# Kernel optimization log

Measured on AMD Instinct MI355X. Metric: run time of the kernel, lower is better.

Reference implementation:

```python
import jax, jax.numpy as jnp
import numpy as np

B, T = 256, 25
PRE = 2048   # resnet feature dim
D = 256      # fc_early_dim = cell_size = in_size = hybrid_in_size
K = 4        # num_atts
NC = 2       # num_classes


def setup_inputs() -> dict:
    key = jax.random.key(0)
    ks = jax.random.split(key, 20)
    def p(k, *s):
        return jax.random.normal(k, s, jnp.float32) * 0.02
    z = lambda *s: jnp.zeros(s, jnp.float32)
    return {
        "x_visual": jax.random.normal(ks[0], (B, T, PRE), jnp.float32),
        "x_tactile": jax.random.normal(ks[1], (B, T, PRE), jnp.float32),
        "fc0_w": p(ks[2], PRE, D), "fc0_b": z(D),
        "fc1_w": p(ks[3], PRE, D), "fc1_b": z(D),
        # LSTHM_V: W(x) + U(h) + V(z), gates packed as [f,i,o,ch]
        "lv_W": p(ks[4], D, 4 * D), "lv_U": p(ks[5], D, 4 * D), "lv_V": p(ks[6], D, 4 * D), "lv_b": z(4 * D),
        # LSTHM_T
        "lt_W": p(ks[7], D, 4 * D), "lt_U": p(ks[8], D, 4 * D), "lt_V": p(ks[9], D, 4 * D), "lt_b": z(4 * D),
        # MAB: attention over concat hidden (2D) producing K attentions
        "att_w": p(ks[10], 2 * D, K * 2 * D), "att_b": z(K * 2 * D),
        "red_v_w": p(ks[11], K * D, D), "red_v_b": z(D),
        "red_t_w": p(ks[12], K * D, D), "red_t_b": z(D),
        "mab_out_w": p(ks[13], 2 * D, D), "mab_out_b": z(D),
        "late0_w": p(ks[14], 2 * D, D), "late0_b": z(D),
        "late1_w": p(ks[15], D, NC), "late1_b": z(NC),
    }


def _lsthm(x, c, h, zz, W, U, V, b):
    s = x @ W + h @ U + zz @ V + b            # [B, 4D]
    f = jax.nn.sigmoid(s[:, :D])
    i = jax.nn.sigmoid(s[:, D:2 * D])
    o = jax.nn.sigmoid(s[:, 2 * D:3 * D])
    ch = jnp.tanh(s[:, 3 * D:])
    c_new = f * c + i * ch
    return c_new, jnp.tanh(c_new) * o


def reference(x_visual, x_tactile, fc0_w, fc0_b, fc1_w, fc1_b,
              lv_W, lv_U, lv_V, lv_b, lt_W, lt_U, lt_V, lt_b,
              att_w, att_b, red_v_w, red_v_b, red_t_w, red_t_b,
              mab_out_w, mab_out_b, late0_w, late0_b, late1_w, late1_b):
    xv = x_visual @ fc0_w + fc0_b             # [B, T, D]
    xt = x_tactile @ fc1_w + fc1_b            # [B, T, D]

    def mab(h_v, h_t):
        h = jnp.concatenate([h_v, h_t], -1)   # [B, 2D]
        att = jax.nn.softmax(h @ att_w + att_b, axis=-1)       # [B, K*2D]
        attd = att.reshape(-1, K, 2 * D) * h[:, None, :]        # K attended copies
        v = attd[:, :, :D].reshape(-1, K * D)
        t = attd[:, :, D:].reshape(-1, K * D)
        rv = jax.nn.relu(v @ red_v_w + red_v_b)
        rt = jax.nn.relu(t @ red_t_w + red_t_b)
        return jnp.concatenate([rv, rt], -1) @ mab_out_w + mab_out_b  # [B, D]

    def step(carry, xs):
        c_v, h_v, c_t, h_t, zz = carry
        xvi, xti = xs
        c_v, h_v = _lsthm(xvi, c_v, h_v, zz, lv_W, lv_U, lv_V, lv_b)
        c_t, h_t = _lsthm(xti, c_t, h_t, zz, lt_W, lt_U, lt_V, lt_b)
        zz = mab(h_v, h_t)
        return (c_v, h_v, c_t, h_t, zz), None

    zeros = jnp.zeros((x_visual.shape[0], D), jnp.float32)
    init = (zeros, zeros, zeros, zeros, zeros)
    (c_v, h_v, c_t, h_t, zz), _ = jax.lax.scan(
        step, init, (jnp.swapaxes(xv, 0, 1), jnp.swapaxes(xt, 0, 1)))
    x = jnp.concatenate([h_v, h_t], -1) @ late0_w + late0_b
    return x @ late1_w + late1_b              # dropout is identity in eval
```

## Files before the change

### kernel.cpp

```cpp
#include <hip/hip_runtime.h>

typedef unsigned short u16;
typedef unsigned int u32;
typedef unsigned long long u64;
using bfrag = __attribute__((ext_vector_type(8))) short;
using facc  = __attribute__((ext_vector_type(4))) float;

#define DEV __device__ __forceinline__
#define AGT __HIP_MEMORY_SCOPE_AGENT

static constexpr size_t o_xv   = 0;
static constexpr size_t o_xt   = 3276800;
static constexpr size_t o_f0T  = 6553600;
static constexpr size_t o_f1T  = 7602176;
static constexpr size_t o_UVWv = 8650752;
static constexpr size_t o_UVWt = 10747904;
static constexpr size_t o_attT = 12845056;
static constexpr size_t o_redT = 14942208;
static constexpr size_t o_bgv  = 15990784;
static constexpr size_t o_bgt  = 15994880;
static constexpr size_t o_mvv  = 15998976;
static constexpr size_t o_mvt  = 16003072;
static constexpr size_t o_FW   = 16007168;
static constexpr size_t o_fb   = 16011264;
static constexpr size_t o_eh   = 16011520;
static constexpr size_t o_psum = 41177344;
static constexpr size_t o_hv   = 42750208;
static constexpr size_t o_ht   = 46158080;
static constexpr size_t o_rvt  = 49565952;
static constexpr size_t o_bar  = 56119552;
static constexpr size_t o_end  = 56135936;

DEV u16 f2bf(float f) {
    u32 u = __float_as_uint(f);
    u32 r = (u + 0x7FFFu + ((u >> 16) & 1u)) >> 16;
    return (u16)r;
}
DEV float bf2f(u16 h) { return __uint_as_float(((u32)h) << 16); }
DEV u32 pk2(float a, float b) { return (u32)f2bf(a) | ((u32)f2bf(b) << 16); }
DEV float sigm(float x) { return 1.0f / (1.0f + __expf(-x)); }
DEV float tanh2(float x) { return 2.0f * sigm(2.0f * x) - 1.0f; }
DEV facc mfma16(bfrag a, bfrag b, facc c) {
    return __builtin_amdgcn_mfma_f32_16x16x32_bf16(a, b, c, 0, 0, 0);
}

DEV void gbar(u32* flags, int b, u32 k) {
    asm volatile("s_waitcnt vmcnt(0)" ::: "memory");
    __syncthreads();
    if (threadIdx.x == 0) {
        __builtin_amdgcn_fence(__ATOMIC_RELEASE, "agent");
        (void)__hip_atomic_exchange(&flags[b * 16], k, __ATOMIC_RELAXED, AGT);
    }
    u32* myf = &flags[threadIdx.x * 16];
    while (__hip_atomic_load(myf, __ATOMIC_RELAXED, AGT) < k)
        __builtin_amdgcn_s_sleep(1);
    __syncthreads();
}


DEV void prep_T(const float* __restrict__ src, u16* dst, int lgK, int N, int nb, int bl, int tid) {
    int pairs = ((1 << lgK) * N) >> 1;
    int kmask = (1 << lgK) - 1;
    for (int idx = bl * 256 + tid; idx < pairs; idx += nb * 256) {
        int i = idx * 2;
        int n = i >> lgK, k = i & kmask;
        *(u32*)&dst[i] = pk2(src[(size_t)k * N + n], src[(size_t)(k + 1) * N + n]);
    }
}

DEV void prep_UVW(const float* U, const float* mo, const float* V, const float* W,
                  u16* dst, int nb, int bl, int tid) {
    for (int idx = bl * 256 + tid; idx < 1024 * 1024; idx += nb * 256) {
        int p = idx >> 10, k = idx & 1023;
        int j = p >> 2, g = p & 3, gc = g * 256 + j;
        float v;
        if (k < 256) v = U[(size_t)k * 1024 + gc];
        else if (k < 768) {
            int s = k - 256;
            float a = 0.f;
            for (int d = 0; d < 256; ++d) a += mo[s * 256 + d] * V[(size_t)d * 1024 + gc];
            v = a;
        } else v = W[(size_t)(k - 768) * 1024 + gc];
        dst[idx] = f2bf(v);
    }
}

DEV void prep_bias(const float* lb, const float* mob, const float* V,
                   float* bg, float* mv, int nb, int bl, int tid) {
    for (int p = bl * 256 + tid; p < 1024; p += nb * 256) {
        int j = p >> 2, g = p & 3, gc = g * 256 + j;
        bg[p] = lb[gc];
        float a = 0.f;
        for (int d = 0; d < 256; ++d) a += mob[d] * V[(size_t)d * 1024 + gc];
        mv[p] = a;
    }
}

DEV void prep_FW(const float* l0w, const float* l0b, const float* l1w, const float* l1b,
                 float* FW, float* fb, int tid) {
    for (int idx = tid; idx < 1024; idx += 256) {
        int k = idx >> 1, c = idx & 1;
        float a = 0.f;
        for (int j = 0; j < 256; ++j) a += l0w[k * 256 + j] * l1w[j * 2 + c];
        FW[idx] = a;
    }
    if (tid < 2) {
        float a = l1b[tid];
        for (int j = 0; j < 256; ++j) a += l0b[j] * l1w[j * 2 + tid];
        fb[tid] = a;
    }
}

struct KP { const float* in[26]; char* ws; float* out; };

__global__ __launch_bounds__(256) void marn_all(KP P) {
    __shared__ __align__(16) unsigned char SM[31744];
    int tid = threadIdx.x, b = blockIdx.x;
    int w = tid >> 6, l = tid & 63, lm = l & 15, kh = l >> 4;
    u32 bk = 0;
    char* ws = P.ws;

    u16* xv = (u16*)(ws + o_xv);
    u16* xt = (u16*)(ws + o_xt);
    u16* f0T = (u16*)(ws + o_f0T);
    u16* f1T = (u16*)(ws + o_f1T);
    u16* UVWv = (u16*)(ws + o_UVWv);
    u16* UVWt = (u16*)(ws + o_UVWt);
    u16* attT = (u16*)(ws + o_attT);
    u16* redT = (u16*)(ws + o_redT);
    float* bgv = (float*)(ws + o_bgv);
    float* bgt = (float*)(ws + o_bgt);
    float* mvv = (float*)(ws + o_mvv);
    float* mvt = (float*)(ws + o_mvt);
    float* FW = (float*)(ws + o_FW);
    float* fb = (float*)(ws + o_fb);
    u16* ehB = (u16*)(ws + o_eh);
    float* psB = (float*)(ws + o_psum);
    u16* hvB = (u16*)(ws + o_hv);
    u16* htB = (u16*)(ws + o_ht);
    u16* rvB = (u16*)(ws + o_rvt);
    u32* bar = (u32*)(ws + o_bar);
    const float* attb = P.in[15];
    const float* rvb = P.in[17];
    const float* rtb = P.in[19];

    if      (b < 24)  prep_T(P.in[2], f0T, 11, 256, 24, b, tid);
    else if (b < 48)  prep_T(P.in[4], f1T, 11, 256, 24, b - 24, tid);
    else if (b < 96)  prep_T(P.in[14], attT, 9, 2048, 48, b - 48, tid);
    else if (b < 108) prep_T(P.in[16], redT, 10, 256, 12, b - 96, tid);
    else if (b < 120) prep_T(P.in[18], redT + 256 * 1024, 10, 256, 12, b - 108, tid);
    else if (b < 176) prep_UVW(P.in[7], P.in[20], P.in[8], P.in[6], UVWv, 56, b - 120, tid);
    else if (b < 232) prep_UVW(P.in[11], P.in[20], P.in[12], P.in[10], UVWt, 56, b - 176, tid);
    else if (b < 236) prep_bias(P.in[9], P.in[21], P.in[8], bgv, mvv, 4, b - 232, tid);
    else if (b < 240) prep_bias(P.in[13], P.in[21], P.in[12], bgt, mvt, 4, b - 236, tid);
    else if (b == 240) prep_FW(P.in[22], P.in[23], P.in[24], P.in[25], FW, fb, tid);
    gbar(bar, b, ++bk);

    {
        u16* Al = (u16*)SM;
        u16* Bl = (u16*)(SM + 9216);
        u16* Lt = (u16*)SM;
        for (int u = b; u < 400; u += 256) {
            int zs = u & 1, ny = (u >> 1) & 1, mx = u >> 2;
            const float* A = zs ? P.in[1] : P.in[0];
            const u16* BT = zs ? f1T : f0T;
            const float* bias = zs ? P.in[5] : P.in[3];
            u16* C = zs ? xt : xv;
            int m0 = mx * 64, n0 = ny * 128;
            int arow = tid >> 2, aseg = tid & 3;
            int brow = tid >> 1, bseg = tid & 1;
            facc acc[8];
#pragma unroll
            for (int i = 0; i < 8; ++i) acc[i] = (facc){0.f, 0.f, 0.f, 0.f};
            for (int c = 0; c < 32; ++c) {
                float4 av[4];
#pragma unroll
                for (int uu = 0; uu < 4; ++uu)
                    av[uu] = *(const float4*)&A[(size_t)(m0 + arow) * 2048 + c * 64 + aseg * 16 + uu * 4];
                uint4 bv[4];
#pragma unroll
                for (int uu = 0; uu < 4; ++uu)
                    bv[uu] = *(const uint4*)&BT[(size_t)(n0 + brow) * 2048 + c * 64 + bseg * 32 + uu * 8];
                __syncthreads();
                u32 pk[8];
#pragma unroll
                for (int uu = 0; uu < 4; ++uu) {
                    pk[2 * uu] = pk2(av[uu].x, av[uu].y);
                    pk[2 * uu + 1] = pk2(av[uu].z, av[uu].w);
                }
                *(uint4*)&Al[arow * 72 + aseg * 16] = make_uint4(pk[0], pk[1], pk[2], pk[3]);
                *(uint4*)&Al[arow * 72 + aseg * 16 + 8] = make_uint4(pk[4], pk[5], pk[6], pk[7]);
#pragma unroll
                for (int uu = 0; uu < 4; ++uu)
                    *(uint4*)&Bl[brow * 72 + bseg * 32 + uu * 8] = bv[uu];
                __syncthreads();
#pragma unroll
                for (int ks = 0; ks < 2; ++ks) {
                    bfrag a = *(const bfrag*)&Al[(16 * w + lm) * 72 + ks * 32 + kh * 8];
#pragma unroll
                    for (int tt = 0; tt < 8; ++tt) {
                        bfrag bb = *(const bfrag*)&Bl[(tt * 16 + lm) * 72 + ks * 32 + kh * 8];
                        acc[tt] = mfma16(a, bb, acc[tt]);
                    }
                }
            }
            __syncthreads();
#pragma unroll
            for (int tt = 0; tt < 8; ++tt)
#pragma unroll
                for (int j = 0; j < 4; ++j)
                    Lt[(16 * w + 4 * kh + j) * 128 + tt * 16 + lm] = f2bf(acc[tt][j] + bias[n0 + tt * 16 + lm]);
            __syncthreads();
            {
                int mloc = tid >> 2, seg = tid & 3;
                int mg = m0 + mloc;
                int bi = mg / 25, ti = mg - bi * 25;
                u16* drow = &C[(size_t)(ti * 256 + bi) * 256 + n0 + seg * 32];
                const uint4* lp = (const uint4*)&Lt[mloc * 128 + seg * 32];
#pragma unroll
                for (int i = 0; i < 4; ++i)
                    *(uint4*)&drow[i * 8] = lp[i];
            }
            __syncthreads();
        }
    }
    gbar(bar, b, ++bk);

    float* sscr = (float*)SM;
    float* ppart = (float*)(SM + 26112);
    float* sinvl = (float*)(SM + 27136);
    float* redscr = (float*)(SM + 27200);
    float creg[2] = {0.f, 0.f};
    int xid = b & 7, q = b >> 3;

    for (int t = 0; t < 25; ++t) {
        const u16* hv_t = hvB + t * 65536;
        const u16* ht_t = htB + t * 65536;
        u16* hv_n = hvB + (t + 1) * 65536;
        u16* ht_n = htB + (t + 1) * 65536;
        const u16* rv_t = rvB + t * 131072;

        {
            int m = q & 3, n = xid * 8 + (q >> 2);
            int r0 = m * 64;
            bool sv = (n < 32);
            int p0 = (sv ? n : n - 32) * 32;
            const u16* UVW = sv ? UVWv : UVWt;
            const u16* hb = sv ? hv_t : ht_t;
            const u16* xb = (sv ? xv : xt) + t * 65536;
            int arow = r0 + 16 * w + lm;
            const u16* Ah = hb + arow * 256 + kh * 8;
            const u16* Ar = rv_t + arow * 512 + kh * 8;
            const u16* Ax = xb + arow * 256 + kh * 8;
            const u16* B0 = UVW + (size_t)(p0 + lm) * 1024 + kh * 8;
            const u16* B1 = UVW + (size_t)(p0 + 16 + lm) * 1024 + kh * 8;
            facc acc0 = (facc){0.f, 0.f, 0.f, 0.f}, acc1 = (facc){0.f, 0.f, 0.f, 0.f};
#pragma unroll
            for (int ks = 0; ks < 8; ++ks) {
                bfrag a = *(const bfrag*)(Ah + ks * 32);
                bfrag b0 = *(const bfrag*)(B0 + ks * 32);
                bfrag b1 = *(const bfrag*)(B1 + ks * 32);
                acc0 = mfma16(a, b0, acc0);
                acc1 = mfma16(a, b1, acc1);
            }
#pragma unroll
            for (int ks = 0; ks < 16; ++ks) {
                bfrag a = *(const bfrag*)(Ar + ks * 32);
                bfrag b0 = *(const bfrag*)(B0 + 256 + ks * 32);
                bfrag b1 = *(const bfrag*)(B1 + 256 + ks * 32);
                acc0 = mfma16(a, b0, acc0);
                acc1 = mfma16(a, b1, acc1);
            }
#pragma unroll
            for (int ks = 0; ks < 8; ++ks) {
                bfrag a = *(const bfrag*)(Ax + ks * 32);
                bfrag b0 = *(const bfrag*)(B0 + 768 + ks * 32);
                bfrag b1 = *(const bfrag*)(B1 + 768 + ks * 32);
                acc0 = mfma16(a, b0, acc0);
                acc1 = mfma16(a, b1, acc1);
            }
            __syncthreads();
#pragma unroll
            for (int j = 0; j < 4; ++j) {
                sscr[(16 * w + 4 * kh + j) * 33 + lm] = acc0[j];
                sscr[(16 * w + 4 * kh + j) * 33 + 16 + lm] = acc1[j];
            }
            __syncthreads();
            const float* bg = sv ? bgv : bgt;
            const float* mv = sv ? mvv : mvt;
            float tf = (t > 0) ? 1.0f : 0.0f;
            int r = tid >> 2, jp = tid & 3;
            float h2[2];
#pragma unroll
            for (int e = 0; e < 2; ++e) {
                int p = jp * 8 + e * 4;
                float4 b4 = *(const float4*)&bg[p0 + p];
                float4 m4 = *(const float4*)&mv[p0 + p];
                float s0 = sscr[r * 33 + p + 0] + b4.x + tf * m4.x;
                float s1 = sscr[r * 33 + p + 1] + b4.y + tf * m4.y;
                float s2 = sscr[r * 33 + p + 2] + b4.z + tf * m4.z;
                float s3 = sscr[r * 33 + p + 3] + b4.w + tf * m4.w;
                float fg = sigm(s0), ig = sigm(s1), og = sigm(s2), ch = tanh2(s3);
                float cn = fg * creg[e] + ig * ch;
                creg[e] = cn;
                h2[e] = tanh2(cn) * og;
            }
            u16* hw = sv ? hv_n : ht_n;
            *(u32*)&hw[(r0 + r) * 256 + (p0 >> 2) + jp * 2] = pk2(h2[0], h2[1]);
        }
        gbar(bar, b, ++bk);

        if (t < 24) {
            u16* eh_t = ehB + (size_t)t * 524288;
            float* ps_t = psB + t * 16384;

            {
                int m = q & 3, n = xid * 8 + (q >> 2);
                int r0 = m * 64, c0 = n * 32;
                int arow = r0 + 16 * w + lm;
                const u16* A0 = hv_n + arow * 256 + kh * 8;
                const u16* A1 = ht_n + arow * 256 + kh * 8;
                const u16* B0 = attT + (size_t)(c0 + lm) * 512 + kh * 8;
                const u16* B1 = attT + (size_t)(c0 + 16 + lm) * 512 + kh * 8;
                facc acc0 = (facc){0.f, 0.f, 0.f, 0.f}, acc1 = (facc){0.f, 0.f, 0.f, 0.f};
#pragma unroll
                for (int ks = 0; ks < 8; ++ks) {
                    bfrag a = *(const bfrag*)(A0 + ks * 32);
                    bfrag b0 = *(const bfrag*)(B0 + ks * 32);
                    bfrag b1 = *(const bfrag*)(B1 + ks * 32);
                    acc0 = mfma16(a, b0, acc0);
                    acc1 = mfma16(a, b1, acc1);
                }
#pragma unroll
                for (int ks = 0; ks < 8; ++ks) {
                    bfrag a = *(const bfrag*)(A1 + ks * 32);
                    bfrag b0 = *(const bfrag*)(B0 + 256 + ks * 32);
                    bfrag b1 = *(const bfrag*)(B1 + 256 + ks * 32);
                    acc0 = mfma16(a, b0, acc0);
                    acc1 = mfma16(a, b1, acc1);
                }
                __syncthreads();
#pragma unroll
                for (int j = 0; j < 4; ++j) {
                    sscr[(16 * w + 4 * kh + j) * 33 + lm] = acc0[j];
                    sscr[(16 * w + 4 * kh + j) * 33 + 16 + lm] = acc1[j];
                }
                __syncthreads();
                int r = tid >> 2, qq = tid & 3;
                int n15 = n & 15;
                const u16* hfs = (n15 < 8) ? hv_n : ht_n;
                int hc0 = (32 * n15) & 255;
                uint4 hfv = *(const uint4*)&hfs[(r0 + r) * 256 + hc0 + qq * 8];
                const u16* hfp = (const u16*)&hfv;
                float ps = 0.f;
                u32 pk[4];
#pragma unroll
                for (int x = 0; x < 4; ++x) {
                    float e0 = __expf(sscr[r * 33 + qq * 8 + 2 * x] + attb[c0 + qq * 8 + 2 * x]);
                    float e1 = __expf(sscr[r * 33 + qq * 8 + 2 * x + 1] + attb[c0 + qq * 8 + 2 * x + 1]);
                    ps += e0 + e1;
                    pk[x] = (u32)f2bf(e0 * bf2f(hfp[2 * x])) | ((u32)f2bf(e1 * bf2f(hfp[2 * x + 1])) << 16);
                }
                *(uint4*)&eh_t[(size_t)(r0 + r) * 2048 + c0 + qq * 8] = make_uint4(pk[0], pk[1], pk[2], pk[3]);
                ppart[r * 4 + qq] = ps;
                __syncthreads();
                if (tid < 64)
                    ps_t[n * 256 + r0 + tid] =
                        ppart[tid * 4] + ppart[tid * 4 + 1] + ppart[tid * 4 + 2] + ppart[tid * 4 + 3];
            }
            gbar(bar, b, ++bk);

            {
                int m = b & 15, n = b >> 4;
                int r0 = m * 16, nc0 = n * 32;
                int half = (n < 8) ? 0 : 1;
                if (tid < 64) {
                    int r = tid >> 2, qq = tid & 3;
                    float s = 0.f;
                    for (int j2 = qq * 16; j2 < qq * 16 + 16; ++j2) s += ps_t[j2 * 256 + r0 + r];
                    ppart[r * 4 + qq] = s;
                }
                __syncthreads();
                if (tid < 16)
                    sinvl[tid] = 1.0f / (ppart[tid * 4] + ppart[tid * 4 + 1] + ppart[tid * 4 + 2] + ppart[tid * 4 + 3]);
                int tt = w & 1, kh2 = w >> 1;
                const u16* Ab = eh_t + (size_t)(r0 + lm) * 2048 + half * 256 + kh * 8;
                const u16* Bb = redT + (size_t)(nc0 + tt * 16 + lm) * 1024 + kh * 8;
                facc acc = (facc){0.f, 0.f, 0.f, 0.f};
#pragma unroll
                for (int s = 0; s < 16; ++s) {
                    int ks = kh2 * 16 + s;
                    int kk = ks * 32;
                    int j = ((kk >> 8) << 9) + (kk & 255);
                    bfrag a = *(const bfrag*)(Ab + j);
                    bfrag bb = *(const bfrag*)(Bb + kk);
                    acc = mfma16(a, bb, acc);
                }
                __syncthreads();
                if (w >= 2) {
#pragma unroll
                    for (int j = 0; j < 4; ++j)
                        redscr[tt * 272 + (4 * kh + j) * 17 + lm] = acc[j];
                }
                __syncthreads();
                if (w < 2) {
#pragma unroll
                    for (int j = 0; j < 4; ++j) {
                        float v = acc[j] + redscr[tt * 272 + (4 * kh + j) * 17 + lm];
                        int rloc = 4 * kh + j;
                        int col = nc0 + tt * 16 + lm;
                        float bs = (col < 256) ? rvb[col] : rtb[col - 256];
                        v = fmaxf(sinvl[rloc] * v + bs, 0.0f);
                        sscr[rloc * 33 + tt * 16 + lm] = v;
                    }
                }
                __syncthreads();
                if (tid < 64) {
                    int rloc = tid >> 2, cp = tid & 3;
                    u16* rw = rvB + (size_t)(t + 1) * 131072;
                    u32 q0 = pk2(sscr[rloc * 33 + cp * 8 + 0], sscr[rloc * 33 + cp * 8 + 1]);
                    u32 q1 = pk2(sscr[rloc * 33 + cp * 8 + 2], sscr[rloc * 33 + cp * 8 + 3]);
                    u32 q2 = pk2(sscr[rloc * 33 + cp * 8 + 4], sscr[rloc * 33 + cp * 8 + 5]);
                    u32 q3 = pk2(sscr[rloc * 33 + cp * 8 + 6], sscr[rloc * 33 + cp * 8 + 7]);
                    *(uint4*)&rw[(size_t)(r0 + rloc) * 512 + nc0 + cp * 8] = make_uint4(q0, q1, q2, q3);
                }
            }
            gbar(bar, b, ++bk);
        }
    }

    {
        const u16* hv25 = hvB + 25 * 65536;
        const u16* ht25 = htB + 25 * 65536;
        if (tid < 64) {
            float a0 = 0.f, a1 = 0.f;
            u64 hv = *(const u64*)&hv25[b * 256 + tid * 4];
            u64 ht = *(const u64*)&ht25[b * 256 + tid * 4];
#pragma unroll
            for (int i = 0; i < 4; ++i) {
                int k = tid * 4 + i;
                float h0 = bf2f((u16)(hv >> (16 * i)));
                float h1 = bf2f((u16)(ht >> (16 * i)));
                a0 += h0 * FW[k * 2] + h1 * FW[(256 + k) * 2];
                a1 += h0 * FW[k * 2 + 1] + h1 * FW[(256 + k) * 2 + 1];
            }
            ppart[tid] = a0;
            ppart[64 + tid] = a1;
        }
        __syncthreads();
        if (tid < 2) {
            float s = fb[tid];
            for (int i = 0; i < 64; ++i) s += ppart[tid * 64 + i];
            P.out[b * 2 + tid] = s;
        }
    }
}


extern "C" void kernel_launch(void* const* d_in, const int* in_sizes, int n_in,
                              void* d_out, int out_size, void* d_ws, size_t ws_size,
                              hipStream_t stream) {
    (void)in_sizes; (void)n_in; (void)out_size; (void)ws_size;
    KP P;
    for (int i = 0; i < 26; ++i) P.in[i] = (const float*)d_in[i];
    P.ws = (char*)d_ws;
    P.out = (float*)d_out;

    hipMemsetAsync((char*)d_ws + o_bar, 0, o_end - o_bar, stream);
    hipMemsetAsync((char*)d_ws + o_hv, 0, 131072, stream);
    hipMemsetAsync((char*)d_ws + o_ht, 0, 131072, stream);
    hipMemsetAsync((char*)d_ws + o_rvt, 0, 262144, stream);

    void* kargs[] = { &P };
    hipError_t e = hipLaunchCooperativeKernel((void*)marn_all, dim3(256), dim3(256),
                                              kargs, 0, stream);
    if (e != hipSuccess) {
        (void)hipGetLastError();
        marn_all<<<dim3(256), dim3(256), 0, stream>>>(P);
    }
}
```

Measured before the change: 1.952 ms.

## Use write-through stores and drop release fence from hot grid barriers

Cross-block data written inside the recurrent loop now goes through inline-asm global stores with sc0 sc1 cache bits, which on gfx94x-class parts write through to a coherent level. This lets the per-step grid barriers skip the agent-scope release fence, which may flush or write back L2. Barrier polling is also spread so 64 lanes each check four flags instead of all 256 threads checking one. Only the first barrier after weight prep keeps the fence. The risk is memory-ordering correctness if any cross-block store is missed or the cache-bit semantics differ on this chip.

New measurement: 1.728 ms. 1.13x faster.

```diff
diff --git a/kernel.cpp b/kernel.cpp
--- a/kernel.cpp
+++ b/kernel.cpp
@@ -5,6 +5,7 @@
 typedef unsigned long long u64;
 using bfrag = __attribute__((ext_vector_type(8))) short;
 using facc  = __attribute__((ext_vector_type(4))) float;
+using u32x4 = __attribute__((ext_vector_type(4))) unsigned int;
 
 #define DEV __device__ __forceinline__
 #define AGT __HIP_MEMORY_SCOPE_AGENT
@@ -44,16 +45,53 @@
     return __builtin_amdgcn_mfma_f32_16x16x32_bf16(a, b, c, 0, 0, 0);
 }
 
+DEV void stwt32(void* p, u32 v) {
+    asm volatile("global_store_dword %0, %1, off sc0 sc1" :: "v"(p), "v"(v) : "memory");
+}
+DEV void stwt128(void* p, u32x4 v) {
+    asm volatile("global_store_dwordx4 %0, %1, off sc0 sc1" :: "v"(p), "v"(v) : "memory");
+}
+DEV void stwtf(float* p, float v) { stwt32((void*)p, __float_as_uint(v)); }
+
 DEV void gbar(u32* flags, int b, u32 k) {
     asm volatile("s_waitcnt vmcnt(0)" ::: "memory");
     __syncthreads();
-    if (threadIdx.x == 0) {
+    int tid = threadIdx.x;
+    if (tid == 0)
+        (void)__hip_atomic_exchange(&flags[b * 16], k, __ATOMIC_RELAXED, AGT);
+    if (tid < 64) {
+        u32* f0 = &flags[tid * 16];
+        u32* f1 = &flags[(tid + 64) * 16];
+        u32* f2 = &flags[(tid + 128) * 16];
+        u32* f3 = &flags[(tid + 192) * 16];
+        while (__hip_atomic_load(f0, __ATOMIC_RELAXED, AGT) < k ||
+               __hip_atomic_load(f1, __ATOMIC_RELAXED, AGT) < k ||
+               __hip_atomic_load(f2, __ATOMIC_RELAXED, AGT) < k ||
+               __hip_atomic_load(f3, __ATOMIC_RELAXED, AGT) < k)
+            __builtin_amdgcn_s_sleep(1);
+    }
+    __syncthreads();
+}
+
+DEV void gbar_fence(u32* flags, int b, u32 k) {
+    asm volatile("s_waitcnt vmcnt(0)" ::: "memory");
+    __syncthreads();
+    int tid = threadIdx.x;
+    if (tid == 0) {
         __builtin_amdgcn_fence(__ATOMIC_RELEASE, "agent");
         (void)__hip_atomic_exchange(&flags[b * 16], k, __ATOMIC_RELAXED, AGT);
     }
-    u32* myf = &flags[threadIdx.x * 16];
-    while (__hip_atomic_load(myf, __ATOMIC_RELAXED, AGT) < k)
-        __builtin_amdgcn_s_sleep(1);
+    if (tid < 64) {
+        u32* f0 = &flags[tid * 16];
+        u32* f1 = &flags[(tid + 64) * 16];
+        u32* f2 = &flags[(tid + 128) * 16];
+        u32* f3 = &flags[(tid + 192) * 16];
+        while (__hip_atomic_load(f0, __ATOMIC_RELAXED, AGT) < k ||
+               __hip_atomic_load(f1, __ATOMIC_RELAXED, AGT) < k ||
+               __hip_atomic_load(f2, __ATOMIC_RELAXED, AGT) < k ||
+               __hip_atomic_load(f3, __ATOMIC_RELAXED, AGT) < k)
+            __builtin_amdgcn_s_sleep(1);
+    }
     __syncthreads();
 }
 
@@ -154,7 +192,7 @@
     else if (b < 236) prep_bias(P.in[9], P.in[21], P.in[8], bgv, mvv, 4, b - 232, tid);
     else if (b < 240) prep_bias(P.in[13], P.in[21], P.in[12], bgt, mvt, 4, b - 236, tid);
     else if (b == 240) prep_FW(P.in[22], P.in[23], P.in[24], P.in[25], FW, fb, tid);
-    gbar(bar, b, ++bk);
+    gbar_fence(bar, b, ++bk);
 
     {
         u16* Al = (u16*)SM;
@@ -216,10 +254,10 @@
                 int mg = m0 + mloc;
                 int bi = mg / 25, ti = mg - bi * 25;
                 u16* drow = &C[(size_t)(ti * 256 + bi) * 256 + n0 + seg * 32];
-                const uint4* lp = (const uint4*)&Lt[mloc * 128 + seg * 32];
+                const u32x4* lp = (const u32x4*)&Lt[mloc * 128 + seg * 32];
 #pragma unroll
                 for (int i = 0; i < 4; ++i)
-                    *(uint4*)&drow[i * 8] = lp[i];
+                    stwt128(&drow[i * 8], lp[i]);
             }
             __syncthreads();
         }
@@ -306,7 +344,7 @@
                 h2[e] = tanh2(cn) * og;
             }
             u16* hw = sv ? hv_n : ht_n;
-            *(u32*)&hw[(r0 + r) * 256 + (p0 >> 2) + jp * 2] = pk2(h2[0], h2[1]);
+            stwt32(&hw[(r0 + r) * 256 + (p0 >> 2) + jp * 2], pk2(h2[0], h2[1]));
         }
         gbar(bar, b, ++bk);
 
@@ -361,12 +399,12 @@
                     ps += e0 + e1;
                     pk[x] = (u32)f2bf(e0 * bf2f(hfp[2 * x])) | ((u32)f2bf(e1 * bf2f(hfp[2 * x + 1])) << 16);
                 }
-                *(uint4*)&eh_t[(size_t)(r0 + r) * 2048 + c0 + qq * 8] = make_uint4(pk[0], pk[1], pk[2], pk[3]);
+                stwt128(&eh_t[(size_t)(r0 + r) * 2048 + c0 + qq * 8], (u32x4){pk[0], pk[1], pk[2], pk[3]});
                 ppart[r * 4 + qq] = ps;
                 __syncthreads();
                 if (tid < 64)
-                    ps_t[n * 256 + r0 + tid] =
-                        ppart[tid * 4] + ppart[tid * 4 + 1] + ppart[tid * 4 + 2] + ppart[tid * 4 + 3];
+                    stwtf(&ps_t[n * 256 + r0 + tid],
+                          ppart[tid * 4] + ppart[tid * 4 + 1] + ppart[tid * 4 + 2] + ppart[tid * 4 + 3]);
             }
             gbar(bar, b, ++bk);
 
@@ -422,7 +460,7 @@
                     u32 q1 = pk2(sscr[rloc * 33 + cp * 8 + 2], sscr[rloc * 33 + cp * 8 + 3]);
                     u32 q2 = pk2(sscr[rloc * 33 + cp * 8 + 4], sscr[rloc * 33 + cp * 8 + 5]);
                     u32 q3 = pk2(sscr[rloc * 33 + cp * 8 + 6], sscr[rloc * 33 + cp * 8 + 7]);
-                    *(uint4*)&rw[(size_t)(r0 + rloc) * 512 + nc0 + cp * 8] = make_uint4(q0, q1, q2, q3);
+                    stwt128(&rw[(size_t)(r0 + rloc) * 512 + nc0 + cp * 8], (u32x4){q0, q1, q2, q3});
                 }
             }
             gbar(bar, b, ++bk);
@@ -466,10 +504,10 @@
     P.ws = (char*)d_ws;
     P.out = (float*)d_out;
 
-    hipMemsetAsync((char*)d_ws + o_bar, 0, o_end - o_bar, stream);
-    hipMemsetAsync((char*)d_ws + o_hv, 0, 131072, stream);
-    hipMemsetAsync((char*)d_ws + o_ht, 0, 131072, stream);
-    hipMemsetAsync((char*)d_ws + o_rvt, 0, 262144, stream);
+    (void)hipMemsetAsync((char*)d_ws + o_bar, 0, o_end - o_bar, stream);
+    (void)hipMemsetAsync((char*)d_ws + o_hv, 0, 131072, stream);
+    (void)hipMemsetAsync((char*)d_ws + o_ht, 0, 131072, stream);
+    (void)hipMemsetAsync((char*)d_ws + o_rvt, 0, 262144, stream);
 
     void* kargs[] = { &P };
     hipError_t e = hipLaunchCooperativeKernel((void*)marn_all, dim3(256), dim3(256),
```
